# Kernel tuning notes

Measured on AMD Instinct MI355X. Metric: run time of the kernel, lower is better.

Reference implementation:

```python
import jax, jax.numpy as jnp
import numpy as np

N = 8000      # num_nodes
U = 64        # num_units
D = 2         # input_dim
K = 2         # max_diffusion_step
E = 64000     # edges per support
B = 32        # batch
F = D + U     # concat feature size = 66
M = 2 * K + 1 # num_matrices = 5


def setup_inputs() -> dict:
    key = jax.random.key(0)
    ks = jax.random.split(key, 10)
    return {
        "inputs": jax.random.normal(ks[0], (B, N * D), dtype=jnp.float32),
        "hx": jax.random.normal(ks[1], (B, N * U), dtype=jnp.float32),
        "row0": jax.random.randint(ks[2], (E,), 0, N, dtype=jnp.int32),
        "col0": jax.random.randint(ks[3], (E,), 0, N, dtype=jnp.int32),
        "val0": jax.random.uniform(ks[4], (E,), dtype=jnp.float32) / 8.0,
        "row1": jax.random.randint(ks[5], (E,), 0, N, dtype=jnp.int32),
        "col1": jax.random.randint(ks[6], (E,), 0, N, dtype=jnp.int32),
        "val1": jax.random.uniform(ks[7], (E,), dtype=jnp.float32) / 8.0,
        "W_ru": jax.random.normal(ks[8], (F * M, 2 * U), dtype=jnp.float32) * 0.05,
        "b_ru": jnp.ones((2 * U,), dtype=jnp.float32),  # bias_start=1.0
        "W_c": jax.random.normal(ks[9], (F * M, U), dtype=jnp.float32) * 0.05,
        "b_c": jnp.zeros((U,), dtype=jnp.float32),       # bias_start=0.0
    }


def _spmm(row, col, val, x):
    # y[r] += val_e * x[c]  for each edge e=(r,c); x: [N, F*B]
    return jax.ops.segment_sum(val[:, None] * x[col], row, num_segments=N)


def _gconv(inputs, state, W, b, supports, output_size):
    # inputs: [B, N*D_in], state: [B, N*D_st]
    x = jnp.concatenate([inputs.reshape(B, N, -1), state.reshape(B, N, -1)], axis=2)  # [B,N,F]
    f = x.shape[2]
    x0 = x.transpose(1, 2, 0).reshape(N, f * B)  # [N, F*B]
    xs = [x0]
    for (row, col, val) in supports:
        x1 = _spmm(row, col, val, x0)
        xs.append(x1)
        xk_1, xk_2 = x1, x0
        for _ in range(2, K + 1):
            x2 = 2.0 * _spmm(row, col, val, xk_1) - xk_2
            xs.append(x2)
            xk_1, xk_2 = x2, xk_1
    m = len(xs)
    # [M,N,F,B] -> [B,N,F,M] -> [B*N, F*M]
    xc = jnp.stack(xs).reshape(m, N, f, B).transpose(3, 1, 2, 0).reshape(B * N, f * m)
    out = xc @ W + b
    return out.reshape(B, N * output_size)


def reference(inputs, hx, row0, col0, val0, row1, col1, val1, W_ru, b_ru, W_c, b_c):
    supports = ((row0, col0, val0), (row1, col1, val1))
    # reset/update gates via graph convolution
    value = jax.nn.sigmoid(_gconv(inputs, hx, W_ru, b_ru, supports, 2 * U))
    value = value.reshape(B, N, 2 * U)
    r = value[..., :U].reshape(B, N * U)
    u = value[..., U:].reshape(B, N * U)
    c = jnp.tanh(_gconv(inputs, r * hx, W_c, b_c, supports, U))
    new_state = u * hx + (1.0 - u) * c
    return new_state
```

## Files before the change

kernel.cpp:

```cpp
#include <hip/hip_runtime.h>
#include <stdint.h>

#define NN 8000
#define UU 64
#define EE 64000
#define BB 32
#define NB 256000
#define HXS 512000

typedef __attribute__((ext_vector_type(8))) __bf16 bf16x8;
typedef __attribute__((ext_vector_type(4))) float f32x4;
typedef __attribute__((ext_vector_type(4))) unsigned int u32x4;
typedef __attribute__((ext_vector_type(2))) unsigned int u32x2;

__device__ __forceinline__ unsigned short f2bf(float f){
  unsigned int u = __builtin_bit_cast(unsigned int, f);
  u += 0x7fffu + ((u >> 16) & 1u);
  return (unsigned short)(u >> 16);
}
__device__ __forceinline__ unsigned int pack2(float a, float b){
  return (unsigned int)f2bf(a) | ((unsigned int)f2bf(b) << 16);
}
__device__ __forceinline__ float bflo(unsigned int w){ return __builtin_bit_cast(float, w << 16); }
__device__ __forceinline__ float bfhi(unsigned int w){ return __builtin_bit_cast(float, w & 0xffff0000u); }
__device__ __forceinline__ float bfu(unsigned short v){ return __builtin_bit_cast(float, (unsigned int)v << 16); }

__device__ __forceinline__ void acc8(float* a, float v, uint4 q){
  a[0]+=v*bflo(q.x); a[1]+=v*bfhi(q.x); a[2]+=v*bflo(q.y); a[3]+=v*bfhi(q.y);
  a[4]+=v*bflo(q.z); a[5]+=v*bfhi(q.z); a[6]+=v*bflo(q.w); a[7]+=v*bfhi(q.w);
}

__device__ __forceinline__ void stage16(const unsigned short* g, unsigned short* ldsbase){
  __builtin_amdgcn_global_load_lds((const __attribute__((address_space(1))) void*)g,
                                   (__attribute__((address_space(3))) void*)ldsbase, 16, 0, 0);
}

__device__ __forceinline__ void ntstore16(uint4 v, uint4* p){
  u32x4 ov = {v.x, v.y, v.z, v.w};
  __builtin_nontemporal_store(ov, (u32x4*)p);
}
__device__ __forceinline__ void ntstore8(uint2 v, uint2* p){
  u32x2 ov = {v.x, v.y};
  __builtin_nontemporal_store(ov, (u32x2*)p);
}

__global__ void k_hist(const int* __restrict__ r0, const int* __restrict__ r1, int* __restrict__ cnt){
  int i = blockIdx.x * 256 + threadIdx.x;
  if (i < 2*EE){
    int s = (i >= EE);
    int r = s ? r1[i - EE] : r0[i];
    atomicAdd(&cnt[s*NN + r], 1);
  }
}

__global__ __launch_bounds__(1024) void k_scan(const int* __restrict__ cnt, int* __restrict__ row_ptr, int* __restrict__ rp_work){
  int sup = blockIdx.x;
  const int* c = cnt + sup*NN;
  __shared__ int part[1024];
  int t = threadIdx.x;
  int loc[8]; int s = 0;
  #pragma unroll
  for (int j=0;j<8;j++){ int idx=t*8+j; int v = (idx<NN)? c[idx]:0; loc[j]=s; s+=v; }
  part[t]=s; __syncthreads();
  for (int o=1;o<1024;o<<=1){
    int v = (t>=o)? part[t-o]:0;
    __syncthreads();
    part[t]+=v;
    __syncthreads();
  }
  int pre = (t>0)? part[t-1]:0;
  #pragma unroll
  for (int j=0;j<8;j++){ int idx=t*8+j; if(idx<NN){ int e=pre+loc[j]; row_ptr[sup*(NN+1)+idx]=e; rp_work[sup*NN+idx]=e; } }
  if (t==1023) row_ptr[sup*(NN+1)+NN] = part[1023];
}

__global__ void k_scatter(const int* __restrict__ r0, const int* __restrict__ c0, const float* __restrict__ v0,
                          const int* __restrict__ r1, const int* __restrict__ c1, const float* __restrict__ v1,
                          int* __restrict__ rp_work, uint2* __restrict__ edge_s){
  int i = blockIdx.x * 256 + threadIdx.x;
  if (i < 2*EE){
    int s = (i >= EE);
    int e = s ? i - EE : i;
    int r  = s ? r1[e] : r0[e];
    int cc = s ? c1[e] : c0[e];
    float vv = s ? v1[e] : v0[e];
    int pos = atomicAdd(&rp_work[s*NN + r], 1);
    uint2 ev; ev.x = (unsigned int)cc; ev.y = __builtin_bit_cast(unsigned int, vv);
    edge_s[s*EE + pos] = ev;
  }
}

__global__ void k_wpack(const float* __restrict__ W_ru, const float* __restrict__ W_c,
                        unsigned short* __restrict__ Wru_t, unsigned short* __restrict__ Wc_t){
  int i = blockIdx.x * 256 + threadIdx.x;
  int k = i / 192; int oo = i % 192;
  const float* W; int ld, NC; unsigned short* dst; int c;
  if (oo < 128){ W = W_ru; ld = 128; NC = 128; dst = Wru_t; c = oo; }
  else         { W = W_c;  ld = 64;  NC = 64;  dst = Wc_t;  c = oo - 128; }
  int o = 4*(c & 15) + ((c >> 4) & 3);
  int wcol = (c >= 64) ? 64 + o : o;
  float v = 0.f;
  if (k < 330){
    int m, fb;
    if (k < 320){ m = k >> 6; fb = (2 + (k & 63)) * 5; }
    else        { int j = k - 320; m = j >> 1; fb = (j & 1) * 5; }
    if      (m==0) v = W[(fb+0)*ld+wcol] - W[(fb+2)*ld+wcol] - W[(fb+4)*ld+wcol];
    else if (m==1) v = W[(fb+1)*ld+wcol];
    else if (m==2) v = 2.f*W[(fb+2)*ld+wcol];
    else if (m==3) v = W[(fb+3)*ld+wcol];
    else           v = 2.f*W[(fb+4)*ld+wcol];
  }
  int dstoff;
  if (k < 320) dstoff = (k>>6)*NC*64 + c*64 + (k&63);
  else         dstoff = 320*NC + c*32 + (k-320);
  dst[dstoff] = f2bf(v);
}

__global__ void k_x0(const float* __restrict__ inputs, const float* __restrict__ hx,
                     uint4* __restrict__ xs0q, unsigned int* __restrict__ xi0){
  int n = blockIdx.x, t = threadIdx.x;
  int b = t >> 3, ug = t & 7;
  const float4 h0 = *(const float4*)(hx + (size_t)b*HXS + n*64 + ug*8);
  const float4 h1 = *(const float4*)(hx + (size_t)b*HXS + n*64 + ug*8 + 4);
  uint4 o;
  o.x = pack2(h0.x, h0.y); o.y = pack2(h0.z, h0.w);
  o.z = pack2(h1.x, h1.y); o.w = pack2(h1.z, h1.w);
  xs0q[((size_t)n*32 + b)*8 + ug] = o;
  if (t < 32){
    int bb = t;
    const float2 g = *(const float2*)(inputs + (size_t)bb*(NN*2) + n*2);
    xi0[(((size_t)(bb>>2)*NN) + n)*4 + (bb&3)] = pack2(g.x, g.y);
  }
}

template<bool WITH_IN>
__global__ __launch_bounds__(256) void k_spmm(const int* __restrict__ row_ptr, const uint2* __restrict__ edge_s,
                                              unsigned short* xsS, uint4* xi4,
                                              int supE0, int msrc0, int mdst0,
                                              int supE1, int msrc1, int mdst1){
  int bid = blockIdx.x;
  if (WITH_IN && bid >= 32000){
    int b2 = bid - 32000;
    int s = b2 & 7, si = (b2 >> 3) & 1, chunk = b2 >> 4;
    int n = chunk*256 + threadIdx.x;
    if (n >= NN) return;
    int supE = si ? supE1 : supE0;
    int msrc = si ? msrc1 : msrc0;
    int mdst = si ? mdst1 : mdst0;
    size_t sb = (size_t)(msrc*8 + s)*NN, db = (size_t)(mdst*8 + s)*NN;
    int beg = row_ptr[supE*(NN+1)+n], end = row_ptr[supE*(NN+1)+n+1];
    const uint2* es = edge_s + supE*EE;
    float ai[8] = {0.f,0.f,0.f,0.f,0.f,0.f,0.f,0.f};
    for (int e = beg; e < end; ++e){
      uint2 ev = es[e];
      float v = __builtin_bit_cast(float, ev.y);
      uint4 qi = xi4[sb + ev.x];
      acc8(ai, v, qi);
    }
    uint4 oi;
    oi.x = pack2(ai[0],ai[1]); oi.y = pack2(ai[2],ai[3]); oi.z = pack2(ai[4],ai[5]); oi.w = pack2(ai[6],ai[7]);
    ntstore16(oi, &xi4[db + n]);
    return;
  }
  int g = __builtin_amdgcn_readfirstlane(bid*4 + (threadIdx.x >> 6));
  int w = g / 8000;
  int n = g - w*8000;
  int slice = w >> 1;
  int si = w & 1;
  int supE = si ? supE1 : supE0;
  int msrc = si ? msrc1 : msrc0;
  int mdst = si ? mdst1 : mdst0;
  int lane = threadIdx.x & 63;
  int off = slice*256 + lane*4;
  const unsigned short* srcS = xsS + (size_t)msrc*(NN*2048);
  unsigned short* dstS = xsS + (size_t)mdst*(NN*2048);
  int beg = __builtin_amdgcn_readfirstlane(row_ptr[supE*(NN+1)+n]);
  int end = __builtin_amdgcn_readfirstlane(row_ptr[supE*(NN+1)+n+1]);
  const uint2* es = edge_s + supE*EE;

  float a0=0.f, a1=0.f, a2=0.f, a3=0.f;
  int e = beg;
  for (; e + 2 <= end; e += 2){
    uint2 ev0 = es[e], ev1 = es[e+1];
    int c0 = __builtin_amdgcn_readfirstlane((int)ev0.x);
    int c1 = __builtin_amdgcn_readfirstlane((int)ev1.x);
    float v0 = __builtin_bit_cast(float, __builtin_amdgcn_readfirstlane(ev0.y));
    float v1 = __builtin_bit_cast(float, __builtin_amdgcn_readfirstlane(ev1.y));
    const unsigned short* rp0 = srcS + (size_t)c0*2048;
    const unsigned short* rp1 = srcS + (size_t)c1*2048;
    uint2 q0 = *(const uint2*)(rp0 + off);
    uint2 q1 = *(const uint2*)(rp1 + off);
    a0 += v0*bflo(q0.x); a1 += v0*bfhi(q0.x); a2 += v0*bflo(q0.y); a3 += v0*bfhi(q0.y);
    a0 += v1*bflo(q1.x); a1 += v1*bfhi(q1.x); a2 += v1*bflo(q1.y); a3 += v1*bfhi(q1.y);
  }
  if (e < end){
    uint2 ev = es[e];
    int c = __builtin_amdgcn_readfirstlane((int)ev.x);
    float v = __builtin_bit_cast(float, __builtin_amdgcn_readfirstlane(ev.y));
    const unsigned short* rp = srcS + (size_t)c*2048;
    uint2 q = *(const uint2*)(rp + off);
    a0 += v*bflo(q.x); a1 += v*bfhi(q.x); a2 += v*bflo(q.y); a3 += v*bfhi(q.y);
  }
  uint2 o; o.x = pack2(a0, a1); o.y = pack2(a2, a3);
  ntstore8(o, (uint2*)(dstS + (size_t)n*2048 + off));
}

template<int NCOL, bool IS_RU>
__global__ __launch_bounds__(256, IS_RU ? 4 : 6) void k_gemm(unsigned short* xsS,
                                                 const unsigned int* __restrict__ xsI,
                                                 const unsigned short* __restrict__ Wp,
                                                 const float* __restrict__ bias,
                                                 const float* __restrict__ hx,
                                                 float* cout,
                                                 unsigned short* ubuf){
  constexpr int CF = NCOL / 16;
  __shared__ unsigned short Bl[2][NCOL*64];
  __shared__ unsigned short Bt[NCOL*32];
  const int t = threadIdx.x;
  const int wv = t >> 6;
  const int l = t & 63;
  const int lr = l & 15;
  const int lg = l >> 4;
  const int R0 = blockIdx.x * 128;

  auto stageB = [&](int m, int buf){
    #pragma unroll
    for (int i=0;i<NCOL*8/256;i++){
      int g = t + i*256;
      int rr = g >> 3, c = g & 7;
      const unsigned short* gp = Wp + (size_t)(m*NCOL + rr)*64 + ((c ^ (rr&7)) << 3);
      stage16(gp, &Bl[buf][(size_t)(i*256 + wv*64)*8]);
    }
  };

  size_t abase[2];
  #pragma unroll
  for (int rf=0; rf<2; rf++)
    abase[rf] = (size_t)(R0 + wv*32 + rf*16 + lr)*64;
  auto loadA = [&](int m, uint4* dst){
    #pragma unroll
    for (int ks=0; ks<2; ks++)
      #pragma unroll
      for (int rf=0; rf<2; rf++)
        dst[ks*2+rf] = *(const uint4*)(xsS + (size_t)m*(NN*2048) + abase[rf] + ks*32 + lg*8);
  };

  uint4 aC[4], aN[4];
  loadA(0, aC);
  uint4 aT[2];
  #pragma unroll
  for (int rf=0; rf<2; rf++){
    int row = R0 + wv*32 + rf*16 + lr;
    int n = row >> 5, b = row & 31;
    size_t ib = (((size_t)(b>>2))*NN + n)*4 + (b&3);
    unsigned int q0=0u,q1=0u,q2=0u,q3=0u;
    if (lg == 0){
      q0 = xsI[ib];
      q1 = xsI[(size_t)8*NN*4 + ib];
      q2 = xsI[(size_t)16*NN*4 + ib];
      q3 = xsI[(size_t)24*NN*4 + ib];
    } else if (lg == 1){
      q0 = xsI[(size_t)32*NN*4 + ib];
    }
    uint4 qq; qq.x=q0; qq.y=q1; qq.z=q2; qq.w=q3;
    aT[rf] = qq;
  }
  stageB(0, 0);
  {
    #pragma unroll
    for (int i=0;i<NCOL*4/256;i++){
      int g = t + i*256;
      int rr = g >> 2, c = g & 3;
      const unsigned short* gp = Wp + (size_t)320*NCOL + rr*32 + ((c ^ (rr&3)) << 3);
      stage16(gp, &Bt[(size_t)(i*256 + wv*64)*8]);
    }
  }
  __syncthreads();

  f32x4 acc[2][CF];
  const f32x4 zero = {0.f,0.f,0.f,0.f};
  #pragma unroll
  for (int rf=0; rf<2; rf++)
    #pragma unroll
    for (int cf=0; cf<CF; cf++) acc[rf][cf] = zero;

  #pragma unroll
  for (int m=0; m<5; m++){
    int cur = m & 1;
    if (m < 4){
      stageB(m+1, cur^1);
      loadA(m+1, aN);
    }
    #pragma unroll
    for (int ks=0; ks<2; ks++){
      #pragma unroll
      for (int cf=0; cf<CF; cf++){
        int col = cf*16 + lr;
        int chunk = (ks*4 + lg) ^ (col & 7);
        bf16x8 bv = __builtin_bit_cast(bf16x8, *(const uint4*)(&Bl[cur][col*64 + chunk*8]));
        acc[0][cf] = __builtin_amdgcn_mfma_f32_16x16x32_bf16(__builtin_bit_cast(bf16x8, aC[ks*2+0]), bv, acc[0][cf], 0, 0, 0);
        acc[1][cf] = __builtin_amdgcn_mfma_f32_16x16x32_bf16(__builtin_bit_cast(bf16x8, aC[ks*2+1]), bv, acc[1][cf], 0, 0, 0);
      }
    }
    __syncthreads();
    #pragma unroll
    for (int i=0;i<4;i++) aC[i] = aN[i];
  }

  #pragma unroll
  for (int cf=0; cf<CF; cf++){
    int col = cf*16 + lr;
    int chunk = lg ^ (col & 3);
    bf16x8 bv = __builtin_bit_cast(bf16x8, *(const uint4*)(&Bt[col*32 + chunk*8]));
    acc[0][cf] = __builtin_amdgcn_mfma_f32_16x16x32_bf16(__builtin_bit_cast(bf16x8, aT[0]), bv, acc[0][cf], 0, 0, 0);
    acc[1][cf] = __builtin_amdgcn_mfma_f32_16x16x32_bf16(__builtin_bit_cast(bf16x8, aT[1]), bv, acc[1][cf], 0, 0, 0);
  }

  #pragma unroll
  for (int rf=0; rf<2; rf++){
    #pragma unroll
    for (int reg=0; reg<4; reg++){
      int row = R0 + wv*32 + rf*16 + (lg << 2) + reg;
      int n = row >> 5, b = row & 31;
      size_t rowoff = (size_t)b*HXS + (size_t)n*UU;
      size_t slot0 = (size_t)row*64;
      int o0 = lr << 2;
      if constexpr (IS_RU){
        uint2 hv = *(const uint2*)(xsS + slot0 + o0);
        unsigned short rr4[4], uu4[4];
        #pragma unroll
        for (int cf=0; cf<4; cf++){
          int o = o0 + cf;
          float vr = acc[rf][cf][reg]   + bias[o];
          float vu = acc[rf][cf+4][reg] + bias[64+o];
          float sgr = 1.f/(1.f + __expf(-vr));
          float sgu = 1.f/(1.f + __expf(-vu));
          float h = bfu(((const unsigned short*)&hv)[cf]);
          rr4[cf] = f2bf(sgr * h);
          uu4[cf] = f2bf(sgu);
        }
        *(uint2*)(xsS + slot0 + o0) = *(uint2*)rr4;
        *(uint2*)(ubuf + rowoff + o0) = *(uint2*)uu4;
      } else {
        float4 hv = *(const float4*)(hx + rowoff + o0);
        uint2 uv = *(const uint2*)(ubuf + rowoff + o0);
        float4 ov;
        #pragma unroll
        for (int cf=0; cf<4; cf++){
          float cc = tanhf(acc[rf][cf][reg] + bias[o0+cf]);
          float uu = bfu(((const unsigned short*)&uv)[cf]);
          float h  = ((const float*)&hv)[cf];
          ((float*)&ov)[cf] = uu*h + (1.f - uu)*cc;
        }
        *(float4*)(cout + rowoff + o0) = ov;
      }
    }
  }
}

extern "C" void kernel_launch(void* const* d_in, const int* in_sizes, int n_in,
                              void* d_out, int out_size, void* d_ws, size_t ws_size,
                              hipStream_t stream){
  const float* inputs = (const float*)d_in[0];
  const float* hx     = (const float*)d_in[1];
  const int*   row0   = (const int*)d_in[2];
  const int*   col0   = (const int*)d_in[3];
  const float* val0   = (const float*)d_in[4];
  const int*   row1   = (const int*)d_in[5];
  const int*   col1   = (const int*)d_in[6];
  const float* val1   = (const float*)d_in[7];
  const float* W_ru   = (const float*)d_in[8];
  const float* b_ru   = (const float*)d_in[9];
  const float* W_c    = (const float*)d_in[10];
  const float* b_c    = (const float*)d_in[11];
  float* out = (float*)d_out;

  char* ws = (char*)d_ws;
  size_t off = 0;
  auto alloc = [&](size_t bytes) -> void* {
    void* p = ws + off;
    off += (bytes + 255) & ~(size_t)255;
    return p;
  };
  unsigned short* xsS   = (unsigned short*)alloc((size_t)5*NN*2048*2);
  unsigned int*   xsI   = (unsigned int*)  alloc((size_t)5*8*NN*16);
  unsigned short* u_buf = (unsigned short*)alloc((size_t)NB*64*2);
  unsigned short* Wru_t = (unsigned short*)alloc((size_t)128*352*2);
  unsigned short* Wc_t  = (unsigned short*)alloc((size_t)64*352*2);
  int*   row_ptr = (int*)  alloc(2*(NN+1)*4);
  uint2* edge_s  = (uint2*)alloc((size_t)2*EE*8);
  int*   cnt     = (int*)  alloc(2*NN*4);
  int*   rp_work = (int*)  alloc(2*NN*4);
  (void)ws_size; (void)in_sizes; (void)n_in; (void)out_size;

  hipMemsetAsync(cnt, 0, 2*NN*4, stream);
  k_hist<<<(2*EE + 255)/256, 256, 0, stream>>>(row0, row1, cnt);
  k_scan<<<2, 1024, 0, stream>>>(cnt, row_ptr, rp_work);
  k_scatter<<<(2*EE + 255)/256, 256, 0, stream>>>(row0, col0, val0, row1, col1, val1, rp_work, edge_s);
  k_wpack<<<(352*192)/256, 256, 0, stream>>>(W_ru, W_c, Wru_t, Wc_t);
  k_x0<<<NN, 256, 0, stream>>>(inputs, hx, (uint4*)xsS, (unsigned int*)xsI);

  uint4* xi4 = (uint4*)xsI;

  k_spmm<true ><<<32512, 256, 0, stream>>>(row_ptr, edge_s, xsS, xi4, 0, 0, 1, 1, 0, 3);
  k_spmm<true ><<<32512, 256, 0, stream>>>(row_ptr, edge_s, xsS, xi4, 0, 1, 2, 1, 3, 4);
  k_gemm<128, true><<<2000, 256, 0, stream>>>(xsS, xsI, Wru_t, b_ru, hx, nullptr, u_buf);

  k_spmm<false><<<32000, 256, 0, stream>>>(row_ptr, edge_s, xsS, xi4, 0, 0, 1, 1, 0, 3);
  k_spmm<false><<<32000, 256, 0, stream>>>(row_ptr, edge_s, xsS, xi4, 0, 1, 2, 1, 3, 4);
  k_gemm<64, false><<<2000, 256, 0, stream>>>(xsS, xsI, Wc_t, b_c, hx, out, u_buf);
}
```

Before: 461.3 us.

## Use persistent grid-stride SpMM with slice-major block mapping for L2 locality

Replaces the one-wave-per-(node,slice) launch of 32000 blocks with a persistent grid of 2048 blocks. Each block is pinned to one feature slice and its waves stride over node tasks, so concurrently running waves gather the same slice of source rows, which is meant to improve L2 reuse and cut block launch overhead. The small input-feature SpMM is folded into the same task loop instead of using extra blocks. The GEMM launch bounds are also relaxed to 3 waves per SIMD for both variants, which trades occupancy for more registers.

```diff
diff --git a/kernel.cpp b/kernel.cpp
--- a/kernel.cpp
+++ b/kernel.cpp
@@ -138,75 +138,74 @@
                                               unsigned short* xsS, uint4* xi4,
                                               int supE0, int msrc0, int mdst0,
                                               int supE1, int msrc1, int mdst1){
-  int bid = blockIdx.x;
-  if (WITH_IN && bid >= 32000){
-    int b2 = bid - 32000;
-    int s = b2 & 7, si = (b2 >> 3) & 1, chunk = b2 >> 4;
-    int n = chunk*256 + threadIdx.x;
-    if (n >= NN) return;
-    int supE = si ? supE1 : supE0;
-    int msrc = si ? msrc1 : msrc0;
-    int mdst = si ? mdst1 : mdst0;
-    size_t sb = (size_t)(msrc*8 + s)*NN, db = (size_t)(mdst*8 + s)*NN;
-    int beg = row_ptr[supE*(NN+1)+n], end = row_ptr[supE*(NN+1)+n+1];
-    const uint2* es = edge_s + supE*EE;
-    float ai[8] = {0.f,0.f,0.f,0.f,0.f,0.f,0.f,0.f};
-    for (int e = beg; e < end; ++e){
-      uint2 ev = es[e];
-      float v = __builtin_bit_cast(float, ev.y);
-      uint4 qi = xi4[sb + ev.x];
-      acc8(ai, v, qi);
-    }
-    uint4 oi;
-    oi.x = pack2(ai[0],ai[1]); oi.y = pack2(ai[2],ai[3]); oi.z = pack2(ai[4],ai[5]); oi.w = pack2(ai[6],ai[7]);
-    ntstore16(oi, &xi4[db + n]);
-    return;
-  }
-  int g = __builtin_amdgcn_readfirstlane(bid*4 + (threadIdx.x >> 6));
-  int w = g / 8000;
-  int n = g - w*8000;
-  int slice = w >> 1;
-  int si = w & 1;
-  int supE = si ? supE1 : supE0;
-  int msrc = si ? msrc1 : msrc0;
-  int mdst = si ? mdst1 : mdst0;
-  int lane = threadIdx.x & 63;
-  int off = slice*256 + lane*4;
-  const unsigned short* srcS = xsS + (size_t)msrc*(NN*2048);
-  unsigned short* dstS = xsS + (size_t)mdst*(NN*2048);
-  int beg = __builtin_amdgcn_readfirstlane(row_ptr[supE*(NN+1)+n]);
-  int end = __builtin_amdgcn_readfirstlane(row_ptr[supE*(NN+1)+n+1]);
-  const uint2* es = edge_s + supE*EE;
-
-  float a0=0.f, a1=0.f, a2=0.f, a3=0.f;
-  int e = beg;
-  for (; e + 2 <= end; e += 2){
-    uint2 ev0 = es[e], ev1 = es[e+1];
-    int c0 = __builtin_amdgcn_readfirstlane((int)ev0.x);
-    int c1 = __builtin_amdgcn_readfirstlane((int)ev1.x);
-    float v0 = __builtin_bit_cast(float, __builtin_amdgcn_readfirstlane(ev0.y));
-    float v1 = __builtin_bit_cast(float, __builtin_amdgcn_readfirstlane(ev1.y));
-    const unsigned short* rp0 = srcS + (size_t)c0*2048;
-    const unsigned short* rp1 = srcS + (size_t)c1*2048;
-    uint2 q0 = *(const uint2*)(rp0 + off);
-    uint2 q1 = *(const uint2*)(rp1 + off);
-    a0 += v0*bflo(q0.x); a1 += v0*bfhi(q0.x); a2 += v0*bflo(q0.y); a3 += v0*bfhi(q0.y);
-    a0 += v1*bflo(q1.x); a1 += v1*bfhi(q1.x); a2 += v1*bflo(q1.y); a3 += v1*bfhi(q1.y);
-  }
-  if (e < end){
-    uint2 ev = es[e];
-    int c = __builtin_amdgcn_readfirstlane((int)ev.x);
-    float v = __builtin_bit_cast(float, __builtin_amdgcn_readfirstlane(ev.y));
-    const unsigned short* rp = srcS + (size_t)c*2048;
-    uint2 q = *(const uint2*)(rp + off);
-    a0 += v*bflo(q.x); a1 += v*bfhi(q.x); a2 += v*bflo(q.y); a3 += v*bfhi(q.y);
-  }
-  uint2 o; o.x = pack2(a0, a1); o.y = pack2(a2, a3);
-  ntstore8(o, (uint2*)(dstS + (size_t)n*2048 + off));
+  const int slice = blockIdx.x & 7;
+  const int wslot = (blockIdx.x >> 3)*4 + (threadIdx.x >> 6);
+  const int lane = threadIdx.x & 63;
+  const int off = slice*256 + lane*4;
+  const int NTASK = WITH_IN ? 18000 : 16000;
+
+  for (int task = wslot; task < NTASK; task += 1024){
+    if (task < 16000){
+      int si = (task >= 8000) ? 1 : 0;
+      int n = task - si*8000;
+      int supE = si ? supE1 : supE0;
+      int msrc = si ? msrc1 : msrc0;
+      int mdst = si ? mdst1 : mdst0;
+      const unsigned short* srcS = xsS + (size_t)msrc*(NN*2048);
+      unsigned short* dstS = xsS + (size_t)mdst*(NN*2048);
+      int beg = __builtin_amdgcn_readfirstlane(row_ptr[supE*(NN+1)+n]);
+      int end = __builtin_amdgcn_readfirstlane(row_ptr[supE*(NN+1)+n+1]);
+      const uint2* es = edge_s + supE*EE;
+      float a0=0.f, a1=0.f, a2=0.f, a3=0.f;
+      int e = beg;
+      for (; e + 2 <= end; e += 2){
+        uint2 ev0 = es[e], ev1 = es[e+1];
+        int c0 = __builtin_amdgcn_readfirstlane((int)ev0.x);
+        int c1 = __builtin_amdgcn_readfirstlane((int)ev1.x);
+        float v0 = __builtin_bit_cast(float, __builtin_amdgcn_readfirstlane(ev0.y));
+        float v1 = __builtin_bit_cast(float, __builtin_amdgcn_readfirstlane(ev1.y));
+        uint2 q0 = *(const uint2*)(srcS + (size_t)c0*2048 + off);
+        uint2 q1 = *(const uint2*)(srcS + (size_t)c1*2048 + off);
+        a0 += v0*bflo(q0.x); a1 += v0*bfhi(q0.x); a2 += v0*bflo(q0.y); a3 += v0*bfhi(q0.y);
+        a0 += v1*bflo(q1.x); a1 += v1*bfhi(q1.x); a2 += v1*bflo(q1.y); a3 += v1*bfhi(q1.y);
+      }
+      if (e < end){
+        uint2 ev = es[e];
+        int c = __builtin_amdgcn_readfirstlane((int)ev.x);
+        float v = __builtin_bit_cast(float, __builtin_amdgcn_readfirstlane(ev.y));
+        uint2 q = *(const uint2*)(srcS + (size_t)c*2048 + off);
+        a0 += v*bflo(q.x); a1 += v*bfhi(q.x); a2 += v*bflo(q.y); a3 += v*bfhi(q.y);
+      }
+      uint2 o; o.x = pack2(a0, a1); o.y = pack2(a2, a3);
+      ntstore8(o, (uint2*)(dstS + (size_t)n*2048 + off));
+    } else if (WITH_IN){
+      int it = task - 16000;
+      int s = it & 7;
+      int rest = it >> 3;
+      int si = rest & 1;
+      int n = (rest >> 1)*64 + lane;
+      int supE = si ? supE1 : supE0;
+      int msrc = si ? msrc1 : msrc0;
+      int mdst = si ? mdst1 : mdst0;
+      size_t sb = (size_t)(msrc*8 + s)*NN, db = (size_t)(mdst*8 + s)*NN;
+      int beg = row_ptr[supE*(NN+1)+n], end = row_ptr[supE*(NN+1)+n+1];
+      const uint2* es = edge_s + supE*EE;
+      float ai[8] = {0.f,0.f,0.f,0.f,0.f,0.f,0.f,0.f};
+      for (int e = beg; e < end; ++e){
+        uint2 ev = es[e];
+        float v = __builtin_bit_cast(float, ev.y);
+        uint4 qi = xi4[sb + ev.x];
+        acc8(ai, v, qi);
+      }
+      uint4 oi;
+      oi.x = pack2(ai[0],ai[1]); oi.y = pack2(ai[2],ai[3]); oi.z = pack2(ai[4],ai[5]); oi.w = pack2(ai[6],ai[7]);
+      ntstore16(oi, &xi4[db + n]);
+    }
+  }
 }
 
 template<int NCOL, bool IS_RU>
-__global__ __launch_bounds__(256, IS_RU ? 4 : 6) void k_gemm(unsigned short* xsS,
+__global__ __launch_bounds__(256, 3) void k_gemm(unsigned short* xsS,
                                                  const unsigned int* __restrict__ xsI,
                                                  const unsigned short* __restrict__ Wp,
                                                  const float* __restrict__ bias,
@@ -402,11 +401,11 @@
 
   uint4* xi4 = (uint4*)xsI;
 
-  k_spmm<true ><<<32512, 256, 0, stream>>>(row_ptr, edge_s, xsS, xi4, 0, 0, 1, 1, 0, 3);
-  k_spmm<true ><<<32512, 256, 0, stream>>>(row_ptr, edge_s, xsS, xi4, 0, 1, 2, 1, 3, 4);
+  k_spmm<true ><<<2048, 256, 0, stream>>>(row_ptr, edge_s, xsS, xi4, 0, 0, 1, 1, 0, 3);
+  k_spmm<true ><<<2048, 256, 0, stream>>>(row_ptr, edge_s, xsS, xi4, 0, 1, 2, 1, 3, 4);
   k_gemm<128, true><<<2000, 256, 0, stream>>>(xsS, xsI, Wru_t, b_ru, hx, nullptr, u_buf);
 
-  k_spmm<false><<<32000, 256, 0, stream>>>(row_ptr, edge_s, xsS, xi4, 0, 0, 1, 1, 0, 3);
-  k_spmm<false><<<32000, 256, 0, stream>>>(row_ptr, edge_s, xsS, xi4, 0, 1, 2, 1, 3, 4);
+  k_spmm<false><<<2048, 256, 0, stream>>>(row_ptr, edge_s, xsS, xi4, 0, 0, 1, 1, 0, 3);
+  k_spmm<false><<<2048, 256, 0, stream>>>(row_ptr, edge_s, xsS, xi4, 0, 1, 2, 1, 3, 4);
   k_gemm<64, false><<<2000, 256, 0, stream>>>(xsS, xsI, Wc_t, b_c, hx, out, u_buf);
 }
```

After: 541.4 us. 17.4% more time.
